# Kernel tuning notes

Hardware: AMD Instinct MI355X
Metric: run time of the kernel (lower is better)

## Reference

```python
import jax, jax.numpy as jnp
import numpy as np

B, P, H, V, E, D = 32, 24, 24, 32000, 300, 512


def setup_inputs() -> dict:
    key = jax.random.key(0)
    ks = jax.random.split(key, 16)
    f32 = jnp.float32

    def nrm(k, shape, fan):
        return jax.random.normal(k, shape, f32) / np.sqrt(fan).astype(np.float32)

    return {
        'premise': jax.random.randint(ks[0], (B, P), 0, V),
        'hypothesis': jax.random.randint(ks[1], (B, H), 0, V),
        'embedding': jax.random.normal(ks[2], (V, E), f32),
        'W_ih': nrm(ks[3], (8 * D, 2 * E), 2 * E),
        'W_hh': nrm(ks[4], (8 * D, 2 * D), 2 * D),
        'b_ih': jnp.zeros((8 * D,), f32),
        'b_hh': jnp.zeros((8 * D,), f32),
        'W_ch': nrm(ks[5], (D, 2 * D), 2 * D),
        'b_ch': jnp.zeros((D,), f32),
        'W_cc': nrm(ks[6], (D, 2 * D), 2 * D),
        'b_cc': jnp.zeros((D,), f32),
        'W1': nrm(ks[7], (D, D), D),
        'b1': jnp.zeros((D,), f32),
        'W2': nrm(ks[8], (D, D), D),
        'b2': jnp.zeros((D,), f32),
        'W3': nrm(ks[9], (3, D), D),
        'b3': jnp.zeros((3,), f32),
    }


def reference(premise, hypothesis, embedding, W_ih, W_hh, b_ih, b_hh,
              W_ch, b_ch, W_cc, b_cc, W1, b1, W2, b2, W3, b3):
    prem = embedding[premise]      # [B,P,E]
    hyp = embedding[hypothesis]    # [B,H,E]
    bsz = prem.shape[0]
    d = W_ch.shape[0]
    prem_t = prem.transpose(1, 0, 2)  # [P,B,E]
    hyp_t = hyp.transpose(1, 0, 2)    # [H,B,E]
    zero = jnp.zeros((bsz, d), prem.dtype)

    def lstm_cell(x, h, c):
        # PyTorch LSTMCell gate order: i, f, g, o
        g = x @ W_ih.T + b_ih + h @ W_hh.T + b_hh
        i, f, gg, o = jnp.split(g, 4, axis=-1)
        c2 = jax.nn.sigmoid(f) * c + jax.nn.sigmoid(i) * jnp.tanh(gg)
        h2 = jax.nn.sigmoid(o) * jnp.tanh(c2)
        return h2, c2

    def outer(row, px):
        # row holds (h,c) of the previous premise row (left neighbors), [H,B,D]
        row_h, row_c = row

        def inner(low, ins):
            lh, lc = low                 # lower neighbor (current row, j-1)
            left_h, left_c, hx = ins     # left neighbor (prev row, j) and hyp emb
            x = jnp.concatenate([px, hx], axis=-1)          # [B,2E]
            hcat = jnp.concatenate([left_h, lh], axis=-1)   # [B,2D]
            ccat = jnp.concatenate([left_c, lc], axis=-1)
            oh, oc = lstm_cell(x, hcat, ccat)
            nh = oh @ W_ch.T + b_ch      # condense to [B,D]
            nc = oc @ W_cc.T + b_cc
            return (nh, nc), (nh, nc)

        _, (nrh, nrc) = jax.lax.scan(inner, (zero, zero), (row_h, row_c, hyp_t))
        return (nrh, nrc), None

    hlen = hyp_t.shape[0]
    init = (jnp.zeros((hlen, bsz, d), prem.dtype),
            jnp.zeros((hlen, bsz, d), prem.dtype))
    (row_h, _), _ = jax.lax.scan(outer, init, prem_t)

    h = row_h[-1]                          # h at grid cell (P,H)
    h = jax.nn.relu(h @ W1.T + b1)
    h = jax.nn.relu(h @ W2.T + b2)
    return jax.nn.softmax(h @ W3.T + b3, axis=1)
```

## Files before the change

### kernel.cpp

```cpp
#include <hip/hip_runtime.h>

#define P_   24
#define H_   24
#define E_   300
#define D_   512
#define TWOD 1024
#define G4   4096
#define SMEMB  27648
#define BUFSZ  23040
#define SMEMG2 46080

typedef __attribute__((ext_vector_type(8))) short bf16x8;
typedef __attribute__((ext_vector_type(4))) float f32x4;

__device__ __forceinline__ float bflo(unsigned w) { return __uint_as_float(w << 16); }
__device__ __forceinline__ float bfhi(unsigned w) { return __uint_as_float(w & 0xffff0000u); }
__device__ __forceinline__ unsigned short f2bf(float f) {
    unsigned int x = __float_as_uint(f);
    unsigned int r = (x + 0x7fffu + ((x >> 16) & 1u)) >> 16;
    return (unsigned short)r;
}
__device__ __forceinline__ float sigf(float x) {
    return 1.0f / (1.0f + __expf(-x));
}
__device__ __forceinline__ float tanh_f(float x) {
    return 2.0f / (1.0f + __expf(-2.0f * x)) - 1.0f;
}

#define CFENCE() asm volatile("" ::: "memory")
#define LD8(p)   __hip_atomic_load((const unsigned long long*)(p), __ATOMIC_RELAXED, __HIP_MEMORY_SCOPE_AGENT)
#define ST8(p,v) __hip_atomic_store((unsigned long long*)(p), (unsigned long long)(v), __ATOMIC_RELAXED, __HIP_MEMORY_SCOPE_AGENT)
#define LDF(p)   __hip_atomic_load((const float*)(p), __ATOMIC_RELAXED, __HIP_MEMORY_SCOPE_AGENT)
#define LDU(p)   __hip_atomic_load((const unsigned*)(p), __ATOMIC_RELAXED, __HIP_MEMORY_SCOPE_AGENT)
#define STU(p,v) __hip_atomic_store((unsigned*)(p), (unsigned)(v), __ATOMIC_RELAXED, __HIP_MEMORY_SCOPE_AGENT)
#define STF(p,v) __hip_atomic_store((float*)(p), (float)(v), __ATOMIC_RELAXED, __HIP_MEMORY_SCOPE_AGENT)
#define AADD(p,v) __hip_atomic_fetch_add((unsigned*)(p), (unsigned)(v), __ATOMIC_RELAXED, __HIP_MEMORY_SCOPE_AGENT)

#define OFF_WHHP 0u
#define OFF_WCHB 8388608u
#define OFF_WCCB 9437184u
#define OFF_APRE 10485760u
#define OFF_CPRE 16777216u
#define OFF_PX   23068672u
#define OFF_HX   23560192u
#define OFF_HBB  24051712u
#define OFF_CBF  25624576u
#define OFF_H2B  28770304u
#define OFF_C2B  30343168u
#define OFF_HF   31916032u
#define OFF_T1   33488896u
#define OFF_T2   33554432u
#define OFF_FLG  33619968u
#define OFF_BAR2 33628160u
#define ZERO_BYTES 18432u

__device__ __forceinline__ void p0_body(
        int gt, int stride,
        const int* __restrict__ prem, const int* __restrict__ hyp,
        const float* __restrict__ emb, const float* __restrict__ Whh,
        const float* __restrict__ Wch, const float* __restrict__ Wcc,
        char* __restrict__ wsb) {
    unsigned short* WhhP = (unsigned short*)(wsb + OFF_WHHP);
    unsigned short* WchB = (unsigned short*)(wsb + OFF_WCHB);
    unsigned short* WccB = (unsigned short*)(wsb + OFF_WCCB);
    unsigned short* PX   = (unsigned short*)(wsb + OFF_PX);
    unsigned short* HX   = (unsigned short*)(wsb + OFF_HX);

    for (int idx = gt; idx < 524288; idx += stride) {
        int n = idx >> 7;
        int k8 = (idx & 127) * 8;
        int q = n >> 10, rest = n & 1023;
        int nt = rest >> 5, u = rest & 31;
        int pr = nt * 128 + q * 32 + u;
        const float* s = Whh + (size_t)n * TWOD + k8;
        float4 va = *(const float4*)s, vb = *(const float4*)(s + 4);
        unsigned long long w0 = (unsigned long long)f2bf(va.x)
            | ((unsigned long long)f2bf(va.y) << 16)
            | ((unsigned long long)f2bf(va.z) << 32)
            | ((unsigned long long)f2bf(va.w) << 48);
        unsigned long long w1 = (unsigned long long)f2bf(vb.x)
            | ((unsigned long long)f2bf(vb.y) << 16)
            | ((unsigned long long)f2bf(vb.z) << 32)
            | ((unsigned long long)f2bf(vb.w) << 48);
        unsigned short* dp = WhhP + (size_t)pr * TWOD + k8;
        ST8(dp, w0); ST8(dp + 4, w1);
    }
    for (int idx = gt; idx < 131072; idx += stride) {
        int cc = idx & 65535;
        const float* s = ((idx < 65536) ? Wch : Wcc) + (size_t)cc * 8;
        unsigned short* dp = ((idx < 65536) ? WchB : WccB) + (size_t)cc * 8;
        float4 va = *(const float4*)s, vb = *(const float4*)(s + 4);
        unsigned long long w0 = (unsigned long long)f2bf(va.x)
            | ((unsigned long long)f2bf(va.y) << 16)
            | ((unsigned long long)f2bf(va.z) << 32)
            | ((unsigned long long)f2bf(va.w) << 48);
        unsigned long long w1 = (unsigned long long)f2bf(vb.x)
            | ((unsigned long long)f2bf(vb.y) << 16)
            | ((unsigned long long)f2bf(vb.z) << 32)
            | ((unsigned long long)f2bf(vb.w) << 48);
        ST8(dp, w0); ST8(dp + 4, w1);
    }
    for (int idx = gt; idx < 61440; idx += stride) {
        int isH = idx >= 30720 ? 1 : 0;
        int id2 = idx - isH * 30720;
        int rb = id2 / 40, c8 = (id2 % 40) * 8;
        int ri = rb >> 5, rbb = rb & 31;
        int tok = isH ? hyp[rbb * H_ + ri] : prem[rbb * P_ + ri];
        const float* s = emb + (size_t)tok * E_ + c8;
        unsigned short o[8];
        for (int e = 0; e < 8; ++e)
            o[e] = (c8 + e < E_) ? f2bf(s[e]) : (unsigned short)0;
        unsigned long long w0 = (unsigned long long)o[0]
            | ((unsigned long long)o[1] << 16)
            | ((unsigned long long)o[2] << 32)
            | ((unsigned long long)o[3] << 48);
        unsigned long long w1 = (unsigned long long)o[4]
            | ((unsigned long long)o[5] << 16)
            | ((unsigned long long)o[6] << 32)
            | ((unsigned long long)o[7] << 48);
        unsigned short* dp = (isH ? HX : PX) + rb * 320 + c8;
        ST8(dp, w0); ST8(dp + 4, w1);
    }
}

__device__ __forceinline__ void p1_body(
        int q, const float* __restrict__ Wih, const float* __restrict__ bih,
        const float* __restrict__ bhh, char* __restrict__ wsb,
        unsigned char* smem) {
    const unsigned short* PX = (const unsigned short*)(wsb + OFF_PX);
    const unsigned short* HX = (const unsigned short*)(wsb + OFF_HX);
    unsigned short* Apre = (unsigned short*)(wsb + OFF_APRE);
    unsigned short* Cpre = (unsigned short*)(wsb + OFF_CPRE);

    const int t = threadIdx.x;
    const int lane = t & 63, wvi = t >> 6, l16 = lane & 15, quad = lane >> 4;
    const int wm = wvi >> 1, wn = wvi & 1;
    unsigned short (*At)[72] = (unsigned short (*)[72])smem;
    unsigned short (*Bt)[72] = (unsigned short (*)[72])(smem + 9216);

    int x = q & 7, slot = q >> 3;
    int z = slot / 48, rem = slot % 48;
    int ntg = rem / 12, mt = rem % 12;
    int nt = ntg * 8 + x;
    const unsigned short* X = z ? HX : PX;
    int koff = z ? E_ : 0;
    unsigned short* Out = z ? Cpre : Apre;
    f32x4 acc[2][4] = {};
    int arow = t >> 2, acol = (t & 3) * 16;
    int brow = t >> 1, bcol = (t & 1) * 32;
    for (int s = 0; s < 5; ++s) {
        int k0 = s * 64;
        {
            const unsigned short* sp = X + (size_t)(mt * 64 + arow) * 320 + k0 + acol;
            unsigned long long x0 = LD8(sp), x1 = LD8(sp + 4);
            unsigned long long x2 = LD8(sp + 8), x3 = LD8(sp + 12);
            unsigned long long* dst = (unsigned long long*)&At[arow][acol];
            dst[0] = x0; dst[1] = x1; dst[2] = x2; dst[3] = x3;
        }
        {
            int n = nt * 128 + brow;
            const float* wrow = Wih + (size_t)n * (2 * E_) + koff;
            unsigned short* dst = &Bt[brow][bcol];
            for (int c4 = 0; c4 < 8; ++c4) {
                int k = k0 + bcol + c4 * 4;
                if (k < E_) {
                    float4 v = *(const float4*)(wrow + k);
                    dst[c4 * 4 + 0] = f2bf(v.x); dst[c4 * 4 + 1] = f2bf(v.y);
                    dst[c4 * 4 + 2] = f2bf(v.z); dst[c4 * 4 + 3] = f2bf(v.w);
                } else {
                    dst[c4 * 4 + 0] = 0; dst[c4 * 4 + 1] = 0;
                    dst[c4 * 4 + 2] = 0; dst[c4 * 4 + 3] = 0;
                }
            }
        }
        __syncthreads();
        for (int ks = 0; ks < 2; ++ks) {
            bf16x8 a[2], bb[4];
            for (int mi = 0; mi < 2; ++mi)
                a[mi] = *(const bf16x8*)&At[wm * 32 + mi * 16 + l16][ks * 32 + quad * 8];
            for (int ni = 0; ni < 4; ++ni)
                bb[ni] = *(const bf16x8*)&Bt[wn * 64 + ni * 16 + l16][ks * 32 + quad * 8];
            for (int mi = 0; mi < 2; ++mi)
                for (int ni = 0; ni < 4; ++ni)
                    acc[mi][ni] = __builtin_amdgcn_mfma_f32_16x16x32_bf16(
                        a[mi], bb[ni], acc[mi][ni], 0, 0, 0);
        }
        __syncthreads();
    }
    for (int mi = 0; mi < 2; ++mi) {
        int rbase = mt * 64 + wm * 32 + mi * 16 + quad * 4;
        for (int ni = 0; ni < 4; ++ni) {
            int n = nt * 128 + wn * 64 + ni * 16 + l16;
            float bias = z ? 0.0f : (bih[n] + bhh[n]);
            for (int r = 0; r < 4; ++r) {
                float val = acc[mi][ni][r] + bias;
                float pv = __shfl_xor(val, 1);
                if ((lane & 1) == 0) {
                    unsigned w2 = (unsigned)f2bf(val) | ((unsigned)f2bf(pv) << 16);
                    STU(&Out[(size_t)(rbase + r) * G4 + n], w2);
                }
            }
        }
    }
    __syncthreads();
}

__device__ __forceinline__ void gates_job(
        int d, int ncells, int j_lo, int job,
        char* __restrict__ wsb, unsigned char* smem, unsigned* flg) {
    const unsigned short* WhhP = (const unsigned short*)(wsb + OFF_WHHP);
    const unsigned short* Apre = (const unsigned short*)(wsb + OFF_APRE);
    const unsigned short* Cpre = (const unsigned short*)(wsb + OFF_CPRE);
    const unsigned short* HbB  = (const unsigned short*)(wsb + OFF_HBB);
    const float*          Cbf  = (const float*)(wsb + OFF_CBF);
    unsigned short* H2B = (unsigned short*)(wsb + OFF_H2B);
    unsigned short* C2B = (unsigned short*)(wsb + OFF_C2B);

    int x = job & 7, slot = job >> 3;
    int ntg = slot / ncells, c = slot - ntg * ncells;
    int nt = ntg * 8 + x;
    int cj = j_lo + c, ci = d - cj;

    const unsigned short* HpB = HbB + (size_t)((d + 1) & 1) * (H_ * 32 * D_);
    const float* Cp = Cbf + (size_t)((d + 1) & 1) * (H_ * 32 * D_);

    const int t = threadIdx.x;
    const int lane = t & 63, wvi = t >> 6, l16 = lane & 15, quad = lane >> 4;

    f32x4 acc[2][2] = {};
    const int arow = t >> 3, acol = (t & 7) * 8;
    const int brow = t >> 1, bcol = (t & 1) * 32;
    const unsigned short* wsrc = WhhP + (size_t)(nt * 128 + brow) * TWOD + bcol;
    const unsigned short* asrcL =
        (ci > 0) ? HpB + (size_t)(cj * 32 + arow) * D_ : nullptr;
    const unsigned short* asrcD =
        (cj > 0) ? HpB + (size_t)((cj - 1) * 32 + arow) * D_ : nullptr;

    uint4 aPre[16];
    #pragma unroll
    for (int s = 0; s < 16; ++s) {
        int kk = s * 64 + acol;
        const unsigned short* sp =
            (kk < D_) ? (asrcL ? asrcL + kk : nullptr)
                      : (asrcD ? asrcD + (kk - D_) : nullptr);
        if (sp) {
            unsigned long long x0 = LD8(sp), x1 = LD8(sp + 4);
            aPre[s].x = (unsigned)x0; aPre[s].y = (unsigned)(x0 >> 32);
            aPre[s].z = (unsigned)x1; aPre[s].w = (unsigned)(x1 >> 32);
        } else {
            aPre[s].x = 0u; aPre[s].y = 0u; aPre[s].z = 0u; aPre[s].w = 0u;
        }
    }
    CFENCE();

    uint4 bA0, bA1, bA2, bA3, bB0, bB1, bB2, bB3;
    #define LOADBA(s_) do {                                                    \
            const uint4* s4 = (const uint4*)(wsrc + (s_) * 64);                \
            bA0 = s4[0]; bA1 = s4[1]; bA2 = s4[2]; bA3 = s4[3];                \
        } while (0)
    #define LOADBB(s_) do {                                                    \
            const uint4* s4 = (const uint4*)(wsrc + (s_) * 64);                \
            bB0 = s4[0]; bB1 = s4[1]; bB2 = s4[2]; bB3 = s4[3];                \
        } while (0)
    #define STOREA(p_, s_) do {                                                \
            unsigned short (*At_)[72] = (unsigned short (*)[72])(smem + (p_) * BUFSZ); \
            unsigned short (*Bt_)[72] = (unsigned short (*)[72])(smem + (p_) * BUFSZ + 4608); \
            *(uint4*)&At_[arow][acol] = aPre[s_];                              \
            uint4* dp = (uint4*)&Bt_[brow][bcol];                              \
            dp[0] = bA0; dp[1] = bA1; dp[2] = bA2; dp[3] = bA3;                \
        } while (0)
    #define STOREB(p_, s_) do {                                                \
            unsigned short (*At_)[72] = (unsigned short (*)[72])(smem + (p_) * BUFSZ); \
            unsigned short (*Bt_)[72] = (unsigned short (*)[72])(smem + (p_) * BUFSZ + 4608); \
            *(uint4*)&At_[arow][acol] = aPre[s_];                              \
            uint4* dp = (uint4*)&Bt_[brow][bcol];                              \
            dp[0] = bB0; dp[1] = bB1; dp[2] = bB2; dp[3] = bB3;                \
        } while (0)

    LOADBA(0);
    LOADBB(1);
    STOREA(0, 0);
    __syncthreads();
    #pragma unroll
    for (int s = 0; s < 16; ++s) {
        if (s < 14) {
            if ((s & 1) == 0) { LOADBA(s + 2); } else { LOADBB(s + 2); }
        }
        int p = s & 1;
        unsigned short (*At)[72] = (unsigned short (*)[72])(smem + p * BUFSZ);
        unsigned short (*Bt)[72] = (unsigned short (*)[72])(smem + p * BUFSZ + 4608);
        for (int ks = 0; ks < 2; ++ks) {
            bf16x8 a0 = *(const bf16x8*)&At[l16][ks * 32 + quad * 8];
            bf16x8 a1 = *(const bf16x8*)&At[16 + l16][ks * 32 + quad * 8];
            bf16x8 b0 = *(const bf16x8*)&Bt[wvi * 32 + l16][ks * 32 + quad * 8];
            bf16x8 b1 = *(const bf16x8*)&Bt[wvi * 32 + 16 + l16][ks * 32 + quad * 8];
            acc[0][0] = __builtin_amdgcn_mfma_f32_16x16x32_bf16(a0, b0, acc[0][0], 0, 0, 0);
            acc[0][1] = __builtin_amdgcn_mfma_f32_16x16x32_bf16(a0, b1, acc[0][1], 0, 0, 0);
            acc[1][0] = __builtin_amdgcn_mfma_f32_16x16x32_bf16(a1, b0, acc[1][0], 0, 0, 0);
            acc[1][1] = __builtin_amdgcn_mfma_f32_16x16x32_bf16(a1, b1, acc[1][1], 0, 0, 0);
        }
        if (s < 15) {
            if ((s & 1) == 0) { STOREB(1 - p, s + 1); } else { STOREA(1 - p, s + 1); }
            __syncthreads();
        }
    }
    #undef LOADBA
    #undef LOADBB
    #undef STOREA
    #undef STOREB

    float* Dt = (float*)smem;
    for (int mi = 0; mi < 2; ++mi)
        for (int ni = 0; ni < 2; ++ni) {
            int cc2 = wvi * 32 + ni * 16 + l16;
            int rr = mi * 16 + quad * 4;
            for (int r = 0; r < 4; ++r)
                Dt[(rr + r) * 132 + cc2] = acc[mi][ni][r];
        }
    __syncthreads();
    {
        int u2 = (t & 15) * 2, r0 = (t >> 4) * 2;
        int k = nt * 32 + u2;
        for (int r = r0; r < r0 + 2; ++r) {
            size_t ai = (size_t)(ci * 32 + r) * G4 + k;
            size_t cix = (size_t)(cj * 32 + r) * G4 + k;
            unsigned ap0 = *(const unsigned*)&Apre[ai];
            unsigned ap1 = *(const unsigned*)&Apre[ai + 1024];
            unsigned ap2 = *(const unsigned*)&Apre[ai + 2048];
            unsigned ap3 = *(const unsigned*)&Apre[ai + 3072];
            unsigned cp0 = *(const unsigned*)&Cpre[cix];
            unsigned cp1 = *(const unsigned*)&Cpre[cix + 1024];
            unsigned cp2 = *(const unsigned*)&Cpre[cix + 2048];
            unsigned cp3 = *(const unsigned*)&Cpre[cix + 3072];
            float ccat0, ccat1;
            if (k < D_) {
                if (ci > 0) {
                    const float* cp = Cp + (size_t)(cj * 32 + r) * D_ + k;
                    ccat0 = LDF(cp); ccat1 = LDF(cp + 1);
                } else { ccat0 = 0.0f; ccat1 = 0.0f; }
            } else {
                if (cj > 0) {
                    const float* cp = Cp + (size_t)((cj - 1) * 32 + r) * D_ + (k - D_);
                    ccat0 = LDF(cp); ccat1 = LDF(cp + 1);
                } else { ccat0 = 0.0f; ccat1 = 0.0f; }
            }
            float g00 = Dt[r * 132 +      u2]     + bflo(ap0) + bflo(cp0);
            float g01 = Dt[r * 132 +      u2 + 1] + bfhi(ap0) + bfhi(cp0);
            float g10 = Dt[r * 132 + 32 + u2]     + bflo(ap1) + bflo(cp1);
            float g11 = Dt[r * 132 + 32 + u2 + 1] + bfhi(ap1) + bfhi(cp1);
            float g20 = Dt[r * 132 + 64 + u2]     + bflo(ap2) + bflo(cp2);
            float g21 = Dt[r * 132 + 64 + u2 + 1] + bfhi(ap2) + bfhi(cp2);
            float g30 = Dt[r * 132 + 96 + u2]     + bflo(ap3) + bflo(cp3);
            float g31 = Dt[r * 132 + 96 + u2 + 1] + bfhi(ap3) + bfhi(cp3);
            float c20 = sigf(g10) * ccat0 + sigf(g00) * tanh_f(g20);
            float h20 = sigf(g30) * tanh_f(c20);
            float c21 = sigf(g11) * ccat1 + sigf(g01) * tanh_f(g21);
            float h21 = sigf(g31) * tanh_f(c21);
            unsigned hw = (unsigned)f2bf(h20) | ((unsigned)f2bf(h21) << 16);
            unsigned cw = (unsigned)f2bf(c20) | ((unsigned)f2bf(c21) << 16);
            STU(&H2B[(size_t)(c * 32 + r) * TWOD + k], hw);
            STU(&C2B[(size_t)(c * 32 + r) * TWOD + k], cw);
        }
    }
    __syncthreads();
    if (t == 0) { CFENCE(); AADD(&flg[c], 1u); CFENCE(); }
}

__device__ __forceinline__ void cond_job(
        int d, int j_lo, int job,
        const float* __restrict__ bch, const float* __restrict__ bcc,
        char* __restrict__ wsb, unsigned char* smem, unsigned* flg) {
    const unsigned short* H2B  = (const unsigned short*)(wsb + OFF_H2B);
    const unsigned short* C2B  = (const unsigned short*)(wsb + OFF_C2B);
    const unsigned short* WchB = (const unsigned short*)(wsb + OFF_WCHB);
    const unsigned short* WccB = (const unsigned short*)(wsb + OFF_WCCB);
    unsigned short* HbB = (unsigned short*)(wsb + OFF_HBB);
    float* Cbf = (float*)(wsb + OFF_CBF);
    float* Hf  = (float*)(wsb + OFF_HF);

    int xcd = job & 7, c = job >> 3;
    int z = xcd >> 2, ntile = xcd & 3;
    const unsigned short* Ain = z ? C2B : H2B;
    const unsigned short* W = z ? WccB : WchB;
    int cj = j_lo + c;

    const int t = threadIdx.x;
    const int lane = t & 63, wvi = t >> 6, l16 = lane & 15, quad = lane >> 4;

    unsigned short* HbC = HbB + (size_t)(d & 1) * (H_ * 32 * D_);
    float* CbC = Cbf + (size_t)(d & 1) * (H_ * 32 * D_);

    if (t == 0) {
        CFENCE();
        while (LDU(&flg[c]) < 32u)
            __builtin_amdgcn_s_sleep(1);
        CFENCE();
    }
    __syncthreads();

    f32x4 acc[2][2] = {};
    const int arow = t >> 3, acol = (t & 7) * 8;
    const int brow = t >> 1, bcol = (t & 1) * 32;
    const unsigned short* asrc = Ain + (size_t)(c * 32 + arow) * TWOD + acol;
    const unsigned short* wsrc = W + (size_t)(ntile * 128 + brow) * TWOD + bcol;

    uint4 aPre[16];
    #pragma unroll
    for (int s = 0; s < 16; ++s) {
        unsigned long long x0 = LD8(asrc + s * 64), x1 = LD8(asrc + s * 64 + 4);
        aPre[s].x = (unsigned)x0; aPre[s].y = (unsigned)(x0 >> 32);
        aPre[s].z = (unsigned)x1; aPre[s].w = (unsigned)(x1 >> 32);
    }
    CFENCE();

    uint4 bA0, bA1, bA2, bA3, bB0, bB1, bB2, bB3;
    #define LOADBA(s_) do {                                                    \
            const uint4* s4 = (const uint4*)(wsrc + (s_) * 64);                \
            bA0 = s4[0]; bA1 = s4[1]; bA2 = s4[2]; bA3 = s4[3];                \
        } while (0)
    #define LOADBB(s_) do {                                                    \
            const uint4* s4 = (const uint4*)(wsrc + (s_) * 64);                \
            bB0 = s4[0]; bB1 = s4[1]; bB2 = s4[2]; bB3 = s4[3];                \
        } while (0)
    #define STOREA(p_, s_) do {                                                \
            unsigned short (*At_)[72] = (unsigned short (*)[72])(smem + (p_) * BUFSZ); \
            unsigned short (*Bt_)[72] = (unsigned short (*)[72])(smem + (p_) * BUFSZ + 4608); \
            *(uint4*)&At_[arow][acol] = aPre[s_];                              \
            uint4* dp = (uint4*)&Bt_[brow][bcol];                              \
            dp[0] = bA0; dp[1] = bA1; dp[2] = bA2; dp[3] = bA3;                \
        } while (0)
    #define STOREB(p_, s_) do {                                                \
            unsigned short (*At_)[72] = (unsigned short (*)[72])(smem + (p_) * BUFSZ); \
            unsigned short (*Bt_)[72] = (unsigned short (*)[72])(smem + (p_) * BUFSZ + 4608); \
            *(uint4*)&At_[arow][acol] = aPre[s_];                              \
            uint4* dp = (uint4*)&Bt_[brow][bcol];                              \
            dp[0] = bB0; dp[1] = bB1; dp[2] = bB2; dp[3] = bB3;                \
        } while (0)

    LOADBA(0);
    LOADBB(1);
    STOREA(0, 0);
    __syncthreads();
    #pragma unroll
    for (int s = 0; s < 16; ++s) {
        if (s < 14) {
            if ((s & 1) == 0) { LOADBA(s + 2); } else { LOADBB(s + 2); }
        }
        int p = s & 1;
        unsigned short (*At)[72] = (unsigned short (*)[72])(smem + p * BUFSZ);
        unsigned short (*Bt)[72] = (unsigned short (*)[72])(smem + p * BUFSZ + 4608);
        for (int ks = 0; ks < 2; ++ks) {
            bf16x8 a0 = *(const bf16x8*)&At[l16][ks * 32 + quad * 8];
            bf16x8 a1 = *(const bf16x8*)&At[16 + l16][ks * 32 + quad * 8];
            bf16x8 b0 = *(const bf16x8*)&Bt[wvi * 32 + l16][ks * 32 + quad * 8];
            bf16x8 b1 = *(const bf16x8*)&Bt[wvi * 32 + 16 + l16][ks * 32 + quad * 8];
            acc[0][0] = __builtin_amdgcn_mfma_f32_16x16x32_bf16(a0, b0, acc[0][0], 0, 0, 0);
            acc[0][1] = __builtin_amdgcn_mfma_f32_16x16x32_bf16(a0, b1, acc[0][1], 0, 0, 0);
            acc[1][0] = __builtin_amdgcn_mfma_f32_16x16x32_bf16(a1, b0, acc[1][0], 0, 0, 0);
            acc[1][1] = __builtin_amdgcn_mfma_f32_16x16x32_bf16(a1, b1, acc[1][1], 0, 0, 0);
        }
        if (s < 15) {
            if ((s & 1) == 0) { STOREB(1 - p, s + 1); } else { STOREA(1 - p, s + 1); }
            __syncthreads();
        }
    }
    #undef LOADBA
    #undef LOADBB
    #undef STOREA
    #undef STOREB

    for (int mi = 0; mi < 2; ++mi) {
        int rr = mi * 16 + quad * 4;
        for (int ni = 0; ni < 2; ++ni) {
            int n = ntile * 128 + wvi * 32 + ni * 16 + l16;
            float bsv = z ? bcc[n] : bch[n];
            for (int r = 0; r < 4; ++r) {
                int rb = rr + r;
                float val = acc[mi][ni][r] + bsv;
                if (z) {
                    STF(&CbC[(size_t)(cj * 32 + rb) * D_ + n], val);
                } else {
                    float pv = __shfl_xor(val, 1);
                    if ((lane & 1) == 0) {
                        unsigned w2 = (unsigned)f2bf(val) | ((unsigned)f2bf(pv) << 16);
                        STU(&HbC[(size_t)(cj * 32 + rb) * D_ + n], w2);
                    }
                    if (d == P_ + H_ - 2)
                        STF(&Hf[(size_t)(cj * 32 + rb) * D_ + n], val);
                }
            }
        }
    }
    __syncthreads();
}

__device__ __forceinline__ void fc_job(
        const float* __restrict__ hin, const float* __restrict__ W,
        const float* __restrict__ bias, float* __restrict__ outv, int job,
        float* hsh) {
    int t = threadIdx.x;
    int row = job >> 1, cb = (job & 1) * 256;
    const float* h = hin + (size_t)row * D_;
    hsh[t * 2]     = LDF(h + t * 2);
    hsh[t * 2 + 1] = LDF(h + t * 2 + 1);
    __syncthreads();
    int col = cb + t;
    const float* w = W + (size_t)col * D_;
    float accv = bias[col];
    for (int k = 0; k < D_; k += 4) {
        float4 wv4 = *(const float4*)(w + k);
        float4 hv = *(const float4*)(hsh + k);
        accv += hv.x * wv4.x + hv.y * wv4.y + hv.z * wv4.z + hv.w * wv4.w;
    }
    STF(&outv[(size_t)row * D_ + col], fmaxf(accv, 0.0f));
    __syncthreads();
}

__device__ __forceinline__ void sm_job(
        const float* __restrict__ T2, const float* __restrict__ W3,
        const float* __restrict__ b3, float* __restrict__ out, float* lg) {
    int t = threadIdx.x;
    if (t < 96) {
        int rb = t / 3, cls = t % 3;
        const float* h = T2 + (size_t)rb * D_;
        const float* w = W3 + (size_t)cls * D_;
        float accv = b3[cls];
        for (int k = 0; k < D_; k += 4) {
            float4 wv4 = *(const float4*)(w + k);
            accv += LDF(h + k) * wv4.x + LDF(h + k + 1) * wv4.y +
                    LDF(h + k + 2) * wv4.z + LDF(h + k + 3) * wv4.w;
        }
        lg[rb * 3 + cls] = accv;
    }
    __syncthreads();
    if (t < 32) {
        float a = lg[t * 3 + 0], bq = lg[t * 3 + 1], cq = lg[t * 3 + 2];
        float m = fmaxf(a, fmaxf(bq, cq));
        float ea = __expf(a - m), eb = __expf(bq - m), ec = __expf(cq - m);
        float s = 1.0f / (ea + eb + ec);
        out[t * 3 + 0] = ea * s;
        out[t * 3 + 1] = eb * s;
        out[t * 3 + 2] = ec * s;
    }
}

__device__ __forceinline__ void gbar(unsigned* bs, unsigned idx, int grid) {
    __syncthreads();
    if (threadIdx.x == 0) {
        unsigned g = blockIdx.x & 31u;
        unsigned gs = (unsigned)grid >> 5;
        CFENCE();
        unsigned old = AADD(bs + g * 32, 1u);
        CFENCE();
        if (old == (idx + 1u) * gs - 1u) {
            unsigned oc = AADD(bs + 1024, 1u);
            CFENCE();
            if (oc == (idx + 1u) * 32u - 1u) {
                #pragma unroll
                for (unsigned gg = 0; gg < 32; ++gg)
                    STU(bs + 1056 + gg * 32, idx + 1u);
            }
        }
        CFENCE();
        while (LDU(bs + 1056 + g * 32) <= idx)
            __builtin_amdgcn_s_sleep(1);
        CFENCE();
    }
    __syncthreads();
}

__global__ __launch_bounds__(256, 3) void k_all(
        const int* __restrict__ prem, const int* __restrict__ hyp,
        const float* __restrict__ emb, const float* __restrict__ Whh,
        const float* __restrict__ Wch, const float* __restrict__ Wcc,
        const float* __restrict__ Wih, const float* __restrict__ bih,
        const float* __restrict__ bhh,
        const float* __restrict__ bch, const float* __restrict__ bcc,
        const float* __restrict__ W1, const float* __restrict__ b1,
        const float* __restrict__ W2, const float* __restrict__ b2,
        const float* __restrict__ W3, const float* __restrict__ b3,
        float* __restrict__ outp, char* __restrict__ wsb) {
    __shared__ __align__(16) unsigned char smem[SMEMG2];
    unsigned* flgA = (unsigned*)(wsb + OFF_FLG);
    unsigned* bs   = (unsigned*)(wsb + OFF_BAR2);
    const int grid = gridDim.x;
    const int gt = blockIdx.x * 256 + threadIdx.x;
    const int gstride = grid * 256;
    unsigned bidx = 0;

    p0_body(gt, gstride, prem, hyp, emb, Whh, Wch, Wcc, wsb);
    gbar(bs, bidx++, grid);
    for (int job = blockIdx.x; job < 768; job += grid)
        p1_body(job, Wih, bih, bhh, wsb, smem);
    gbar(bs, bidx++, grid);

    for (int d = 0; d < P_ + H_ - 1; ++d) {
        int j_lo = (d > P_ - 1) ? d - (P_ - 1) : 0;
        int j_hi = (d < H_ - 1) ? d : H_ - 1;
        int ncells = j_hi - j_lo + 1;
        unsigned* flg = flgA + d * H_;
        for (int job = blockIdx.x; job < ncells * 32; job += grid)
            gates_job(d, ncells, j_lo, job, wsb, smem, flg);
        for (int job = blockIdx.x; job < ncells * 8; job += grid)
            cond_job(d, j_lo, job, bch, bcc, wsb, smem, flg);
        gbar(bs, bidx++, grid);
    }
    const float* hfin = (const float*)(wsb + OFF_HF) + (size_t)(H_ - 1) * 32 * D_;
    float* T1 = (float*)(wsb + OFF_T1);
    float* T2 = (float*)(wsb + OFF_T2);
    if (blockIdx.x < 64) fc_job(hfin, W1, b1, T1, blockIdx.x, (float*)smem);
    gbar(bs, bidx++, grid);
    if (blockIdx.x < 64) fc_job(T1, W2, b2, T2, blockIdx.x, (float*)smem);
    gbar(bs, bidx++, grid);
    if (blockIdx.x == 0) sm_job(T2, W3, b3, outp, (float*)smem);
}

__global__ __launch_bounds__(256) void k_p0(
        const int* __restrict__ prem, const int* __restrict__ hyp,
        const float* __restrict__ emb, const float* __restrict__ Whh,
        const float* __restrict__ Wch, const float* __restrict__ Wcc,
        char* __restrict__ wsb) {
    p0_body(blockIdx.x * 256 + threadIdx.x, gridDim.x * 256,
            prem, hyp, emb, Whh, Wch, Wcc, wsb);
}

__global__ __launch_bounds__(256) void k_p1(
        const float* __restrict__ Wih, const float* __restrict__ bih,
        const float* __restrict__ bhh, char* __restrict__ wsb) {
    __shared__ __align__(16) unsigned char smem[SMEMB];
    p1_body(blockIdx.x, Wih, bih, bhh, wsb, smem);
}

__global__ __launch_bounds__(256, 3) void k_gates(int d, int ncells, char* __restrict__ wsb) {
    __shared__ __align__(16) unsigned char smem[SMEMG2];
    int j_lo = (d > P_ - 1) ? d - (P_ - 1) : 0;
    gates_job(d, ncells, j_lo, blockIdx.x, wsb, smem,
              (unsigned*)(wsb + OFF_FLG) + d * H_);
}

__global__ __launch_bounds__(256, 3) void k_cond(
        int d, const float* __restrict__ bch, const float* __restrict__ bcc,
        char* __restrict__ wsb) {
    __shared__ __align__(16) unsigned char smem[SMEMG2];
    int j_lo = (d > P_ - 1) ? d - (P_ - 1) : 0;
    cond_job(d, j_lo, blockIdx.x, bch, bcc, wsb, smem,
             (unsigned*)(wsb + OFF_FLG) + d * H_);
}

__global__ __launch_bounds__(256) void k_fc(
        const float* __restrict__ hin, const float* __restrict__ W,
        const float* __restrict__ bias, float* __restrict__ outv) {
    __shared__ float hsh[512];
    fc_job(hin, W, bias, outv, blockIdx.x, hsh);
}

__global__ __launch_bounds__(128) void k_sm(
        const float* __restrict__ T2, const float* __restrict__ W3,
        const float* __restrict__ b3, float* __restrict__ out) {
    __shared__ float lg[96];
    sm_job(T2, W3, b3, out, lg);
}

extern "C" void kernel_launch(void* const* d_in, const int* in_sizes, int n_in,
                              void* d_out, int out_size, void* d_ws, size_t ws_size,
                              hipStream_t stream) {
    (void)in_sizes; (void)n_in; (void)out_size; (void)ws_size;

    const int* prem = (const int*)d_in[0];
    const int* hyp  = (const int*)d_in[1];
    const float* emb = (const float*)d_in[2];
    const float* Wih = (const float*)d_in[3];
    const float* Whh = (const float*)d_in[4];
    const float* bih = (const float*)d_in[5];
    const float* bhh = (const float*)d_in[6];
    const float* Wch = (const float*)d_in[7];
    const float* bch = (const float*)d_in[8];
    const float* Wcc = (const float*)d_in[9];
    const float* bcc = (const float*)d_in[10];
    const float* W1  = (const float*)d_in[11];
    const float* b1  = (const float*)d_in[12];
    const float* W2  = (const float*)d_in[13];
    const float* b2  = (const float*)d_in[14];
    const float* W3  = (const float*)d_in[15];
    const float* b3  = (const float*)d_in[16];
    float* outp = (float*)d_out;
    char* wsb = (char*)d_ws;

    (void)hipMemsetAsync(wsb + OFF_FLG, 0, ZERO_BYTES, stream);

    bool ok = false;
    {
        int maxb = 0;
        if (hipOccupancyMaxActiveBlocksPerMultiprocessor(
                &maxb, reinterpret_cast<const void*>(k_all), 256, 0) == hipSuccess &&
            maxb > 0) {
            int grid = (maxb >= 3) ? 768 : (maxb == 2 ? 512 : 256);
            void* args[] = {(void*)&prem, (void*)&hyp, (void*)&emb, (void*)&Whh,
                            (void*)&Wch, (void*)&Wcc, (void*)&Wih, (void*)&bih,
                            (void*)&bhh, (void*)&bch, (void*)&bcc,
                            (void*)&W1, (void*)&b1, (void*)&W2, (void*)&b2,
                            (void*)&W3, (void*)&b3, (void*)&outp, (void*)&wsb};
            ok = hipLaunchCooperativeKernel(reinterpret_cast<const void*>(k_all),
                                            dim3(grid), dim3(256), args, 0,
                                            stream) == hipSuccess;
        }
    }
    if (!ok) {
        k_p0<<<512, 256, 0, stream>>>(prem, hyp, emb, Whh, Wch, Wcc, wsb);
        k_p1<<<768, 256, 0, stream>>>(Wih, bih, bhh, wsb);
        for (int d = 0; d < P_ + H_ - 1; ++d) {
            int j_lo = (d > P_ - 1) ? d - (P_ - 1) : 0;
            int j_hi = (d < H_ - 1) ? d : H_ - 1;
            int ncells = j_hi - j_lo + 1;
            k_gates<<<ncells * 32, 256, 0, stream>>>(d, ncells, wsb);
            k_cond<<<ncells * 8, 256, 0, stream>>>(d, bch, bcc, wsb);
        }
        float* T1 = (float*)(wsb + OFF_T1);
        float* T2 = (float*)(wsb + OFF_T2);
        const float* hfin = (const float*)(wsb + OFF_HF) + (size_t)(H_ - 1) * 32 * D_;
        k_fc<<<64, 256, 0, stream>>>(hfin, W1, b1, T1);
        k_fc<<<64, 256, 0, stream>>>(T1, W2, b2, T2);
        k_sm<<<1, 128, 0, stream>>>(T2, W3, b3, outp);
    }
}
```

Measured before the change: 1.898 ms.

## Load MFMA operands directly from global into registers, dropping LDS staging

```diff
diff --git a/kernel.cpp b/kernel.cpp
--- a/kernel.cpp
+++ b/kernel.cpp
@@ -7,8 +7,7 @@
 #define TWOD 1024
 #define G4   4096
 #define SMEMB  27648
-#define BUFSZ  23040
-#define SMEMG2 46080
+#define SMEMD  17024
 
 typedef __attribute__((ext_vector_type(8))) short bf16x8;
 typedef __attribute__((ext_vector_type(4))) float f32x4;
@@ -35,6 +34,12 @@
 #define STU(p,v) __hip_atomic_store((unsigned*)(p), (unsigned)(v), __ATOMIC_RELAXED, __HIP_MEMORY_SCOPE_AGENT)
 #define STF(p,v) __hip_atomic_store((float*)(p), (float)(v), __ATOMIC_RELAXED, __HIP_MEMORY_SCOPE_AGENT)
 #define AADD(p,v) __hip_atomic_fetch_add((unsigned*)(p), (unsigned)(v), __ATOMIC_RELAXED, __HIP_MEMORY_SCOPE_AGENT)
+
+__device__ __forceinline__ bf16x8 lda16(const unsigned short* p) {
+    union { unsigned long long u[2]; bf16x8 v; } w;
+    w.u[0] = LD8(p); w.u[1] = LD8(p + 4);
+    return w.v;
+}
 
 #define OFF_WHHP 0u
 #define OFF_WCHB 8388608u
@@ -227,87 +232,55 @@
     const int t = threadIdx.x;
     const int lane = t & 63, wvi = t >> 6, l16 = lane & 15, quad = lane >> 4;
 
+    const unsigned short* wrow0 = WhhP + (size_t)(nt * 128 + wvi * 32 + l16) * TWOD;
+    const unsigned short* wrow1 = wrow0 + (size_t)16 * TWOD;
+    const unsigned short* aL0 = (ci > 0) ? HpB + (size_t)(cj * 32 + l16) * D_ : nullptr;
+    const unsigned short* aL1 = (ci > 0) ? HpB + (size_t)(cj * 32 + 16 + l16) * D_ : nullptr;
+    const unsigned short* aD0 = (cj > 0) ? HpB + (size_t)((cj - 1) * 32 + l16) * D_ : nullptr;
+    const unsigned short* aD1 = (cj > 0) ? HpB + (size_t)((cj - 1) * 32 + 16 + l16) * D_ : nullptr;
+
+    const bf16x8 kz = {};
     f32x4 acc[2][2] = {};
-    const int arow = t >> 3, acol = (t & 7) * 8;
-    const int brow = t >> 1, bcol = (t & 1) * 32;
-    const unsigned short* wsrc = WhhP + (size_t)(nt * 128 + brow) * TWOD + bcol;
-    const unsigned short* asrcL =
-        (ci > 0) ? HpB + (size_t)(cj * 32 + arow) * D_ : nullptr;
-    const unsigned short* asrcD =
-        (cj > 0) ? HpB + (size_t)((cj - 1) * 32 + arow) * D_ : nullptr;
-
-    uint4 aPre[16];
+    bf16x8 fa00[2], fa01[2], fa10[2], fa11[2];
+    bf16x8 fb00[2], fb01[2], fb10[2], fb11[2];
+
+    #define GAF(r_, co_) \
+        (((co_) < D_) ? ((r_##0_) ? lda16(r_##0_ + (co_)) : kz) \
+                      : ((r_##1_) ? lda16(r_##1_ + ((co_) - D_)) : kz))
+
+    #define GLD(b_, s_) do {                                                   \
+            const int co0 = (s_) * 64 + quad * 8;                              \
+            const int co1 = co0 + 32;                                          \
+            fa00[b_] = (co0 < D_) ? (aL0 ? lda16(aL0 + co0) : kz)              \
+                                  : (aD0 ? lda16(aD0 + co0 - D_) : kz);        \
+            fa01[b_] = (co1 < D_) ? (aL0 ? lda16(aL0 + co1) : kz)              \
+                                  : (aD0 ? lda16(aD0 + co1 - D_) : kz);        \
+            fa10[b_] = (co0 < D_) ? (aL1 ? lda16(aL1 + co0) : kz)              \
+                                  : (aD1 ? lda16(aD1 + co0 - D_) : kz);        \
+            fa11[b_] = (co1 < D_) ? (aL1 ? lda16(aL1 + co1) : kz)              \
+                                  : (aD1 ? lda16(aD1 + co1 - D_) : kz);        \
+            fb00[b_] = *(const bf16x8*)(wrow0 + co0);                          \
+            fb01[b_] = *(const bf16x8*)(wrow0 + co1);                          \
+            fb10[b_] = *(const bf16x8*)(wrow1 + co0);                          \
+            fb11[b_] = *(const bf16x8*)(wrow1 + co1);                          \
+        } while (0)
+
+    GLD(0, 0);
     #pragma unroll
     for (int s = 0; s < 16; ++s) {
-        int kk = s * 64 + acol;
-        const unsigned short* sp =
-            (kk < D_) ? (asrcL ? asrcL + kk : nullptr)
-                      : (asrcD ? asrcD + (kk - D_) : nullptr);
-        if (sp) {
-            unsigned long long x0 = LD8(sp), x1 = LD8(sp + 4);
-            aPre[s].x = (unsigned)x0; aPre[s].y = (unsigned)(x0 >> 32);
-            aPre[s].z = (unsigned)x1; aPre[s].w = (unsigned)(x1 >> 32);
-        } else {
-            aPre[s].x = 0u; aPre[s].y = 0u; aPre[s].z = 0u; aPre[s].w = 0u;
-        }
-    }
-    CFENCE();
-
-    uint4 bA0, bA1, bA2, bA3, bB0, bB1, bB2, bB3;
-    #define LOADBA(s_) do {                                                    \
-            const uint4* s4 = (const uint4*)(wsrc + (s_) * 64);                \
-            bA0 = s4[0]; bA1 = s4[1]; bA2 = s4[2]; bA3 = s4[3];                \
-        } while (0)
-    #define LOADBB(s_) do {                                                    \
-            const uint4* s4 = (const uint4*)(wsrc + (s_) * 64);                \
-            bB0 = s4[0]; bB1 = s4[1]; bB2 = s4[2]; bB3 = s4[3];                \
-        } while (0)
-    #define STOREA(p_, s_) do {                                                \
-            unsigned short (*At_)[72] = (unsigned short (*)[72])(smem + (p_) * BUFSZ); \
-            unsigned short (*Bt_)[72] = (unsigned short (*)[72])(smem + (p_) * BUFSZ + 4608); \
-            *(uint4*)&At_[arow][acol] = aPre[s_];                              \
-            uint4* dp = (uint4*)&Bt_[brow][bcol];                              \
-            dp[0] = bA0; dp[1] = bA1; dp[2] = bA2; dp[3] = bA3;                \
-        } while (0)
-    #define STOREB(p_, s_) do {                                                \
-            unsigned short (*At_)[72] = (unsigned short (*)[72])(smem + (p_) * BUFSZ); \
-            unsigned short (*Bt_)[72] = (unsigned short (*)[72])(smem + (p_) * BUFSZ + 4608); \
-            *(uint4*)&At_[arow][acol] = aPre[s_];                              \
-            uint4* dp = (uint4*)&Bt_[brow][bcol];                              \
-            dp[0] = bB0; dp[1] = bB1; dp[2] = bB2; dp[3] = bB3;                \
-        } while (0)
-
-    LOADBA(0);
-    LOADBB(1);
-    STOREA(0, 0);
-    __syncthreads();
-    #pragma unroll
-    for (int s = 0; s < 16; ++s) {
-        if (s < 14) {
-            if ((s & 1) == 0) { LOADBA(s + 2); } else { LOADBB(s + 2); }
-        }
-        int p = s & 1;
-        unsigned short (*At)[72] = (unsigned short (*)[72])(smem + p * BUFSZ);
-        unsigned short (*Bt)[72] = (unsigned short (*)[72])(smem + p * BUFSZ + 4608);
-        for (int ks = 0; ks < 2; ++ks) {
-            bf16x8 a0 = *(const bf16x8*)&At[l16][ks * 32 + quad * 8];
-            bf16x8 a1 = *(const bf16x8*)&At[16 + l16][ks * 32 + quad * 8];
-            bf16x8 b0 = *(const bf16x8*)&Bt[wvi * 32 + l16][ks * 32 + quad * 8];
-            bf16x8 b1 = *(const bf16x8*)&Bt[wvi * 32 + 16 + l16][ks * 32 + quad * 8];
-            acc[0][0] = __builtin_amdgcn_mfma_f32_16x16x32_bf16(a0, b0, acc[0][0], 0, 0, 0);
-            acc[0][1] = __builtin_amdgcn_mfma_f32_16x16x32_bf16(a0, b1, acc[0][1], 0, 0, 0);
-            acc[1][0] = __builtin_amdgcn_mfma_f32_16x16x32_bf16(a1, b0, acc[1][0], 0, 0, 0);
-            acc[1][1] = __builtin_amdgcn_mfma_f32_16x16x32_bf16(a1, b1, acc[1][1], 0, 0, 0);
-        }
-        if (s < 15) {
-            if ((s & 1) == 0) { STOREB(1 - p, s + 1); } else { STOREA(1 - p, s + 1); }
-            __syncthreads();
-        }
-    }
-    #undef LOADBA
-    #undef LOADBB
-    #undef STOREA
-    #undef STOREB
+        const int c_ = s & 1;
+        if (s < 15) GLD(1 - c_, s + 1);
+        acc[0][0] = __builtin_amdgcn_mfma_f32_16x16x32_bf16(fa00[c_], fb00[c_], acc[0][0], 0, 0, 0);
+        acc[0][1] = __builtin_amdgcn_mfma_f32_16x16x32_bf16(fa00[c_], fb10[c_], acc[0][1], 0, 0, 0);
+        acc[1][0] = __builtin_amdgcn_mfma_f32_16x16x32_bf16(fa10[c_], fb00[c_], acc[1][0], 0, 0, 0);
+        acc[1][1] = __builtin_amdgcn_mfma_f32_16x16x32_bf16(fa10[c_], fb10[c_], acc[1][1], 0, 0, 0);
+        acc[0][0] = __builtin_amdgcn_mfma_f32_16x16x32_bf16(fa01[c_], fb01[c_], acc[0][0], 0, 0, 0);
+        acc[0][1] = __builtin_amdgcn_mfma_f32_16x16x32_bf16(fa01[c_], fb11[c_], acc[0][1], 0, 0, 0);
+        acc[1][0] = __builtin_amdgcn_mfma_f32_16x16x32_bf16(fa11[c_], fb01[c_], acc[1][0], 0, 0, 0);
+        acc[1][1] = __builtin_amdgcn_mfma_f32_16x16x32_bf16(fa11[c_], fb11[c_], acc[1][1], 0, 0, 0);
+    }
+    #undef GLD
+    #undef GAF
 
     float* Dt = (float*)smem;
     for (int mi = 0; mi < 2; ++mi)
@@ -370,6 +343,7 @@
         int d, int j_lo, int job,
         const float* __restrict__ bch, const float* __restrict__ bcc,
         char* __restrict__ wsb, unsigned char* smem, unsigned* flg) {
+    (void)smem;
     const unsigned short* H2B  = (const unsigned short*)(wsb + OFF_H2B);
     const unsigned short* C2B  = (const unsigned short*)(wsb + OFF_C2B);
     const unsigned short* WchB = (const unsigned short*)(wsb + OFF_WCHB);
@@ -398,76 +372,43 @@
     }
     __syncthreads();
 
+    const unsigned short* arow0 = Ain + (size_t)(c * 32 + l16) * TWOD;
+    const unsigned short* arow1 = Ain + (size_t)(c * 32 + 16 + l16) * TWOD;
+    const unsigned short* wrow0 = W + (size_t)(ntile * 128 + wvi * 32 + l16) * TWOD;
+    const unsigned short* wrow1 = wrow0 + (size_t)16 * TWOD;
+
     f32x4 acc[2][2] = {};
-    const int arow = t >> 3, acol = (t & 7) * 8;
-    const int brow = t >> 1, bcol = (t & 1) * 32;
-    const unsigned short* asrc = Ain + (size_t)(c * 32 + arow) * TWOD + acol;
-    const unsigned short* wsrc = W + (size_t)(ntile * 128 + brow) * TWOD + bcol;
-
-    uint4 aPre[16];
+    bf16x8 fa00[2], fa01[2], fa10[2], fa11[2];
+    bf16x8 fb00[2], fb01[2], fb10[2], fb11[2];
+
+    #define CLD(b_, s_) do {                                                   \
+            const int co0 = (s_) * 64 + quad * 8;                              \
+            const int co1 = co0 + 32;                                          \
+            fa00[b_] = lda16(arow0 + co0);                                     \
+            fa01[b_] = lda16(arow0 + co1);                                     \
+            fa10[b_] = lda16(arow1 + co0);                                     \
+            fa11[b_] = lda16(arow1 + co1);                                     \
+            fb00[b_] = *(const bf16x8*)(wrow0 + co0);                          \
+            fb01[b_] = *(const bf16x8*)(wrow0 + co1);                          \
+            fb10[b_] = *(const bf16x8*)(wrow1 + co0);                          \
+            fb11[b_] = *(const bf16x8*)(wrow1 + co1);                          \
+        } while (0)
+
+    CLD(0, 0);
     #pragma unroll
     for (int s = 0; s < 16; ++s) {
-        unsigned long long x0 = LD8(asrc + s * 64), x1 = LD8(asrc + s * 64 + 4);
-        aPre[s].x = (unsigned)x0; aPre[s].y = (unsigned)(x0 >> 32);
-        aPre[s].z = (unsigned)x1; aPre[s].w = (unsigned)(x1 >> 32);
-    }
-    CFENCE();
-
-    uint4 bA0, bA1, bA2, bA3, bB0, bB1, bB2, bB3;
-    #define LOADBA(s_) do {                                                    \
-            const uint4* s4 = (const uint4*)(wsrc + (s_) * 64);                \
-            bA0 = s4[0]; bA1 = s4[1]; bA2 = s4[2]; bA3 = s4[3];                \
-        } while (0)
-    #define LOADBB(s_) do {                                                    \
-            const uint4* s4 = (const uint4*)(wsrc + (s_) * 64);                \
-            bB0 = s4[0]; bB1 = s4[1]; bB2 = s4[2]; bB3 = s4[3];                \
-        } while (0)
-    #define STOREA(p_, s_) do {                                                \
-            unsigned short (*At_)[72] = (unsigned short (*)[72])(smem + (p_) * BUFSZ); \
-            unsigned short (*Bt_)[72] = (unsigned short (*)[72])(smem + (p_) * BUFSZ + 4608); \
-            *(uint4*)&At_[arow][acol] = aPre[s_];                              \
-            uint4* dp = (uint4*)&Bt_[brow][bcol];                              \
-            dp[0] = bA0; dp[1] = bA1; dp[2] = bA2; dp[3] = bA3;                \
-        } while (0)
-    #define STOREB(p_, s_) do {                                                \
-            unsigned short (*At_)[72] = (unsigned short (*)[72])(smem + (p_) * BUFSZ); \
-            unsigned short (*Bt_)[72] = (unsigned short (*)[72])(smem + (p_) * BUFSZ + 4608); \
-            *(uint4*)&At_[arow][acol] = aPre[s_];                              \
-            uint4* dp = (uint4*)&Bt_[brow][bcol];                              \
-            dp[0] = bB0; dp[1] = bB1; dp[2] = bB2; dp[3] = bB3;                \
-        } while (0)
-
-    LOADBA(0);
-    LOADBB(1);
-    STOREA(0, 0);
-    __syncthreads();
-    #pragma unroll
-    for (int s = 0; s < 16; ++s) {
-        if (s < 14) {
-            if ((s & 1) == 0) { LOADBA(s + 2); } else { LOADBB(s + 2); }
-        }
-        int p = s & 1;
-        unsigned short (*At)[72] = (unsigned short (*)[72])(smem + p * BUFSZ);
-        unsigned short (*Bt)[72] = (unsigned short (*)[72])(smem + p * BUFSZ + 4608);
-        for (int ks = 0; ks < 2; ++ks) {
-            bf16x8 a0 = *(const bf16x8*)&At[l16][ks * 32 + quad * 8];
-            bf16x8 a1 = *(const bf16x8*)&At[16 + l16][ks * 32 + quad * 8];
-            bf16x8 b0 = *(const bf16x8*)&Bt[wvi * 32 + l16][ks * 32 + quad * 8];
-            bf16x8 b1 = *(const bf16x8*)&Bt[wvi * 32 + 16 + l16][ks * 32 + quad * 8];
-            acc[0][0] = __builtin_amdgcn_mfma_f32_16x16x32_bf16(a0, b0, acc[0][0], 0, 0, 0);
-            acc[0][1] = __builtin_amdgcn_mfma_f32_16x16x32_bf16(a0, b1, acc[0][1], 0, 0, 0);
-            acc[1][0] = __builtin_amdgcn_mfma_f32_16x16x32_bf16(a1, b0, acc[1][0], 0, 0, 0);
-            acc[1][1] = __builtin_amdgcn_mfma_f32_16x16x32_bf16(a1, b1, acc[1][1], 0, 0, 0);
-        }
-        if (s < 15) {
-            if ((s & 1) == 0) { STOREB(1 - p, s + 1); } else { STOREA(1 - p, s + 1); }
-            __syncthreads();
-        }
-    }
-    #undef LOADBA
-    #undef LOADBB
-    #undef STOREA
-    #undef STOREB
+        const int c_ = s & 1;
+        if (s < 15) CLD(1 - c_, s + 1);
+        acc[0][0] = __builtin_amdgcn_mfma_f32_16x16x32_bf16(fa00[c_], fb00[c_], acc[0][0], 0, 0, 0);
+        acc[0][1] = __builtin_amdgcn_mfma_f32_16x16x32_bf16(fa00[c_], fb10[c_], acc[0][1], 0, 0, 0);
+        acc[1][0] = __builtin_amdgcn_mfma_f32_16x16x32_bf16(fa10[c_], fb00[c_], acc[1][0], 0, 0, 0);
+        acc[1][1] = __builtin_amdgcn_mfma_f32_16x16x32_bf16(fa10[c_], fb10[c_], acc[1][1], 0, 0, 0);
+        acc[0][0] = __builtin_amdgcn_mfma_f32_16x16x32_bf16(fa01[c_], fb01[c_], acc[0][0], 0, 0, 0);
+        acc[0][1] = __builtin_amdgcn_mfma_f32_16x16x32_bf16(fa01[c_], fb11[c_], acc[0][1], 0, 0, 0);
+        acc[1][0] = __builtin_amdgcn_mfma_f32_16x16x32_bf16(fa11[c_], fb01[c_], acc[1][0], 0, 0, 0);
+        acc[1][1] = __builtin_amdgcn_mfma_f32_16x16x32_bf16(fa11[c_], fb11[c_], acc[1][1], 0, 0, 0);
+    }
+    #undef CLD
 
     for (int mi = 0; mi < 2; ++mi) {
         int rr = mi * 16 + quad * 4;
@@ -491,7 +432,6 @@
             }
         }
     }
-    __syncthreads();
 }
 
 __device__ __forceinline__ void fc_job(
@@ -580,7 +520,7 @@
         const float* __restrict__ W2, const float* __restrict__ b2,
         const float* __restrict__ W3, const float* __restrict__ b3,
         float* __restrict__ outp, char* __restrict__ wsb) {
-    __shared__ __align__(16) unsigned char smem[SMEMG2];
+    __shared__ __align__(16) unsigned char smem[SMEMB];
     unsigned* flgA = (unsigned*)(wsb + OFF_FLG);
     unsigned* bs   = (unsigned*)(wsb + OFF_BAR2);
     const int grid = gridDim.x;
@@ -632,7 +572,7 @@
 }
 
 __global__ __launch_bounds__(256, 3) void k_gates(int d, int ncells, char* __restrict__ wsb) {
-    __shared__ __align__(16) unsigned char smem[SMEMG2];
+    __shared__ __align__(16) unsigned char smem[SMEMD];
     int j_lo = (d > P_ - 1) ? d - (P_ - 1) : 0;
     gates_job(d, ncells, j_lo, blockIdx.x, wsb, smem,
               (unsigned*)(wsb + OFF_FLG) + d * H_);
@@ -641,7 +581,7 @@
 __global__ __launch_bounds__(256, 3) void k_cond(
         int d, const float* __restrict__ bch, const float* __restrict__ bcc,
         char* __restrict__ wsb) {
-    __shared__ __align__(16) unsigned char smem[SMEMG2];
+    __shared__ __align__(16) unsigned char smem[64];
     int j_lo = (d > P_ - 1) ? d - (P_ - 1) : 0;
     cond_job(d, j_lo, blockIdx.x, bch, bcc, wsb, smem,
              (unsigned*)(wsb + OFF_FLG) + d * H_);
```

Measured after the change: 3.833 ms. +101.9%, slower.
